# Kernel optimization log

Hardware: AMD Instinct MI355X
Metric: run time of the kernel (lower is better)

## Reference

```python
import jax, jax.numpy as jnp
import numpy as np

B, S, D, H, L, V = 32, 100, 1024, 16, 2, 32000
DF = 4 * D
EPS_LN = 1e-5
EPS_Q = 1e-6


def _ln(x, scale, bias):
    mu = jnp.mean(x, axis=-1, keepdims=True)
    var = jnp.mean(jnp.square(x - mu), axis=-1, keepdims=True)
    return (x - mu) * jax.lax.rsqrt(var + EPS_LN) * scale + bias


def setup_inputs() -> dict:
    key = jax.random.key(0)
    ks = jax.random.split(key, 20)
    sd = 0.02
    inp = {
        "x": jax.random.randint(ks[0], (B, S), 0, V),
        "emb": jax.random.normal(ks[1], (V, D), jnp.float32) * sd,
        "pos_emb": jax.random.normal(ks[2], (100, D), jnp.float32) * sd,
        "qkv_w": jax.random.normal(ks[3], (L, 3 * D, D), jnp.float32) * sd,
        "qkv_b": jnp.zeros((L, 3 * D), jnp.float32),
        "out_w": jax.random.normal(ks[4], (L, D, D), jnp.float32) * sd,
        "out_b": jnp.zeros((L, D), jnp.float32),
        "ln1_s": jnp.ones((L, D), jnp.float32),
        "ln1_b": jnp.zeros((L, D), jnp.float32),
        "ff1_w": jax.random.normal(ks[5], (L, DF, D), jnp.float32) * sd,
        "ff1_b": jnp.zeros((L, DF), jnp.float32),
        "ff2_w": jax.random.normal(ks[6], (L, D, DF), jnp.float32) * sd,
        "ff2_b": jnp.zeros((L, D), jnp.float32),
        "ln2_s": jnp.ones((L, D), jnp.float32),
        "ln2_b": jnp.zeros((L, D), jnp.float32),
        "dec_w": jax.random.normal(ks[7], (V, D), jnp.float32) * sd,
        "dec_b": jnp.zeros((V,), jnp.float32),
    }
    return inp


def reference(x, emb, pos_emb, qkv_w, qkv_b, out_w, out_b, ln1_s, ln1_b,
              ff1_w, ff1_b, ff2_w, ff2_b, ln2_s, ln2_b, dec_w, dec_b):
    hd = D // H
    h = emb[x] + pos_emb[:S][None, :, :]  # [B,S,D]
    for l in range(L):
        qkv = h @ qkv_w[l].T + qkv_b[l]  # [B,S,3D]
        q, k, v = jnp.split(qkv, 3, axis=-1)
        q = q.reshape(B, S, H, hd).transpose(0, 2, 1, 3)
        k = k.reshape(B, S, H, hd).transpose(0, 2, 1, 3)
        v = v.reshape(B, S, H, hd).transpose(0, 2, 1, 3)
        scores = jnp.einsum('bhqd,bhkd->bhqk', q, k) / jnp.sqrt(jnp.float32(hd))
        attn = jax.nn.softmax(scores, axis=-1)
        ctx = jnp.einsum('bhqk,bhkd->bhqd', attn, v)
        ctx = ctx.transpose(0, 2, 1, 3).reshape(B, S, D)
        attn_out = ctx @ out_w[l].T + out_b[l]
        h = _ln(h + attn_out, ln1_s[l], ln1_b[l])  # post-norm
        ff = jax.nn.gelu(h @ ff1_w[l].T + ff1_b[l], approximate=False) @ ff2_w[l].T + ff2_b[l]
        h = _ln(h + ff, ln2_s[l], ln2_b[l])
    # Ternary decoder (faithful to the original pack/unpack semantics:
    # packed code = q+1; unpack adds x when code==1 (q==0) and subtracts when
    # code==2 (q==+1), i.e. effective weight = {q==0: +1, q==+1: -1, q==-1: 0}).
    g = jnp.mean(jnp.abs(dec_w))
    wq = jnp.clip(jnp.round(dec_w / (g + EPS_Q)), -1.0, 1.0)
    w_eff = jnp.where(wq == 0.0, 1.0, jnp.where(wq == 1.0, -1.0, 0.0)).astype(jnp.float32)
    return h @ w_eff.T + dec_b  # [B,S,V]
```

## Files before the change

### kernel.cpp

```cpp
#include <hip/hip_runtime.h>
#include <hip/hip_bf16.h>
#include <math.h>

#define B_ 32
#define S_ 100
#define D_ 1024
#define H_ 16
#define L_ 2
#define V_ 32000
#define DF_ 4096
#define HD_ 64
#define MPAD 3328

typedef __bf16 bf16x8 __attribute__((ext_vector_type(8)));
typedef float f32x4 __attribute__((ext_vector_type(4)));

__device__ __forceinline__ void async_copy16(const void* g, void* l) {
  __builtin_amdgcn_global_load_lds((const __attribute__((address_space(1))) void*)g,
                                   (__attribute__((address_space(3))) void*)l, 16, 0, 0);
}

__global__ void absmean_kernel(const float* __restrict__ w, double* __restrict__ out) {
  const long long n4 = (long long)V_ * D_ / 4;
  double s = 0.0;
  long long stride = (long long)gridDim.x * blockDim.x;
  for (long long i = (long long)blockIdx.x * blockDim.x + threadIdx.x; i < n4; i += stride) {
    float4 v = ((const float4*)w)[i];
    s += (double)fabsf(v.x) + (double)fabsf(v.y) + (double)fabsf(v.z) + (double)fabsf(v.w);
  }
#pragma unroll
  for (int off = 32; off > 0; off >>= 1) s += __shfl_down(s, off);
  __shared__ double sm[4];
  int lane = threadIdx.x & 63, wv = threadIdx.x >> 6;
  if (lane == 0) sm[wv] = s;
  __syncthreads();
  if (threadIdx.x == 0) atomicAdd(out, sm[0] + sm[1] + sm[2] + sm[3]);
}

__global__ void quantize_kernel(const float* __restrict__ w, const double* __restrict__ gsum,
                                __hip_bfloat16* __restrict__ q) {
  const long long n4 = (long long)V_ * D_ / 4;
  double g = (*gsum) / ((double)V_ * D_) + 1e-6;
  double inv_g = 1.0 / g;
  long long stride = (long long)gridDim.x * blockDim.x;
  for (long long i = (long long)blockIdx.x * blockDim.x + threadIdx.x; i < n4; i += stride) {
    float4 v = ((const float4*)w)[i];
    union { __hip_bfloat16 h[4]; uint2 u; } o;
    float vv[4] = {v.x, v.y, v.z, v.w};
#pragma unroll
    for (int j = 0; j < 4; ++j) {
      double r = rint((double)vv[j] * inv_g);
      r = fmin(1.0, fmax(-1.0, r));
      float w_eff = (r == 0.0) ? 1.0f : ((r == 1.0) ? -1.0f : 0.0f);
      o.h[j] = __float2bfloat16(w_eff);
    }
    ((uint2*)q)[i] = o.u;
  }
}

__global__ void cast_all_kernel(const float* __restrict__ qkv_w, const float* __restrict__ out_w,
                                const float* __restrict__ ff1_w, const float* __restrict__ ff2_w,
                                __hip_bfloat16* __restrict__ qd, __hip_bfloat16* __restrict__ od,
                                __hip_bfloat16* __restrict__ f1d, __hip_bfloat16* __restrict__ f2d) {
  const long long n1 = (long long)2 * 3072 * 1024 / 4;
  const long long n2 = n1 + (long long)2 * 1024 * 1024 / 4;
  const long long n3 = n2 + (long long)2 * 4096 * 1024 / 4;
  const long long n4 = n3 + (long long)2 * 1024 * 4096 / 4;
  long long stride = (long long)gridDim.x * blockDim.x;
  for (long long i = (long long)blockIdx.x * blockDim.x + threadIdx.x; i < n4; i += stride) {
    const float* src; __hip_bfloat16* dst; long long j;
    if (i < n1)      { src = qkv_w; dst = qd;  j = i; }
    else if (i < n2) { src = out_w; dst = od;  j = i - n1; }
    else if (i < n3) { src = ff1_w; dst = f1d; j = i - n2; }
    else             { src = ff2_w; dst = f2d; j = i - n3; }
    float4 v = ((const float4*)src)[j];
    union { __hip_bfloat16 h[4]; uint2 u; } o;
    o.h[0] = __float2bfloat16(v.x);
    o.h[1] = __float2bfloat16(v.y);
    o.h[2] = __float2bfloat16(v.z);
    o.h[3] = __float2bfloat16(v.w);
    ((uint2*)dst)[j] = o.u;
  }
}

__global__ __launch_bounds__(256) void embed_kernel(const int* __restrict__ x,
    const float* __restrict__ emb, const float* __restrict__ pos,
    float* __restrict__ h, __hip_bfloat16* __restrict__ hb) {
  int row = blockIdx.x;
  int s = row % S_;
  int tok = x[row];
  size_t eb = (size_t)tok * D_, pb = (size_t)s * D_, hb0 = (size_t)row * D_;
#pragma unroll
  for (int i = 0; i < 4; ++i) {
    int d = threadIdx.x + i * 256;
    float v = emb[eb + d] + pos[pb + d];
    h[hb0 + d] = v;
    hb[hb0 + d] = __float2bfloat16(v);
  }
}

__device__ __forceinline__ float gelu_exact(float v) {
  return 0.5f * v * (1.0f + erff(v * 0.70710678118654752f));
}

template <int ACT, int OUTBF>
__global__ __launch_bounds__(256) void gemm_bf(const __hip_bfloat16* __restrict__ A,
    const __hip_bfloat16* __restrict__ Bm, const float* __restrict__ bias,
    void* __restrict__ C, void* __restrict__ C2, int M, int N, int K, int lda, int ldb) {
  __shared__ __bf16 As[128 * 64];
  __shared__ __bf16 Bs[128 * 64];
  int tid = threadIdx.x;
  int lane = tid & 63, wid = tid >> 6;
  int wr = wid >> 1, wc = wid & 1;
  int z = blockIdx.z;

  int nwg = gridDim.x * gridDim.y;
  int orig = blockIdx.y * gridDim.x + blockIdx.x;
  int q = nwg >> 3, r = nwg & 7;
  int xcd = orig & 7, local = orig >> 3;
  int wgid = (xcd < r ? xcd * (q + 1) : r * (q + 1) + (xcd - r) * q) + local;
  int row0 = (wgid % gridDim.x) * 128;
  int col0 = (wgid / gridDim.x) * 128;

  const __hip_bfloat16* Az = A + (size_t)z * K;
  const __hip_bfloat16* Bz = Bm + (size_t)z * K;
  int j0 = wid * 2;
  const __hip_bfloat16* Ag0 = Az + (size_t)(row0 + j0 * 16 + (lane >> 2)) * lda + (lane & 3) * 8;
  const __hip_bfloat16* Ag1 = Az + (size_t)(row0 + (j0 + 1) * 16 + (lane >> 2)) * lda + (lane & 3) * 8;
  const __hip_bfloat16* Bg0 = Bz + (size_t)(col0 + j0 * 16 + (lane >> 2)) * ldb + (lane & 3) * 8;
  const __hip_bfloat16* Bg1 = Bz + (size_t)(col0 + (j0 + 1) * 16 + (lane >> 2)) * ldb + (lane & 3) * 8;
  __bf16* Al0 = As + j0 * 512;
  __bf16* Al1 = As + (j0 + 1) * 512;
  __bf16* Bl0 = Bs + j0 * 512;
  __bf16* Bl1 = Bs + (j0 + 1) * 512;

  float bias_v[4];
#pragma unroll
  for (int ni = 0; ni < 4; ++ni)
    bias_v[ni] = (z == 0) ? bias[col0 + wc * 64 + ni * 16 + (lane & 15)] : 0.f;

  f32x4 acc[4][4];
#pragma unroll
  for (int mi = 0; mi < 4; ++mi)
#pragma unroll
    for (int ni = 0; ni < 4; ++ni) acc[mi][ni] = (f32x4){0.f, 0.f, 0.f, 0.f};

  const bf16x8* Asv = reinterpret_cast<const bf16x8*>(As);
  const bf16x8* Bsv = reinterpret_cast<const bf16x8*>(Bs);
  int afr = (wr * 64 + (lane & 15)) * 4 + (lane >> 4);
  int bfr = (wc * 64 + (lane & 15)) * 4 + (lane >> 4);

  for (int k0 = 0; k0 < K; k0 += 64) {
    async_copy16(Ag0, Al0);  async_copy16(Ag0 + 32, (char*)Al0 + 8192);
    async_copy16(Ag1, Al1);  async_copy16(Ag1 + 32, (char*)Al1 + 8192);
    async_copy16(Bg0, Bl0);  async_copy16(Bg0 + 32, (char*)Bl0 + 8192);
    async_copy16(Bg1, Bl1);  async_copy16(Bg1 + 32, (char*)Bl1 + 8192);
    Ag0 += 64; Ag1 += 64; Bg0 += 64; Bg1 += 64;
    __syncthreads();
    bf16x8 af[4][2], bq[4][2];
#pragma unroll
    for (int mi = 0; mi < 4; ++mi)
#pragma unroll
      for (int kk = 0; kk < 2; ++kk) af[mi][kk] = Asv[afr + mi * 64 + kk * 512];
#pragma unroll
    for (int ni = 0; ni < 4; ++ni)
#pragma unroll
      for (int kk = 0; kk < 2; ++kk) bq[ni][kk] = Bsv[bfr + ni * 64 + kk * 512];
#pragma unroll
    for (int mi = 0; mi < 4; ++mi)
#pragma unroll
      for (int ni = 0; ni < 4; ++ni)
#pragma unroll
        for (int kk = 0; kk < 2; ++kk)
          acc[mi][ni] = __builtin_amdgcn_mfma_f32_16x16x32_bf16(af[mi][kk], bq[ni][kk], acc[mi][ni], 0, 0, 0);
    __syncthreads();
  }

  float* Cf = (float*)((z == 0) ? C : C2);
  __hip_bfloat16* Cb = (__hip_bfloat16*)C;
#pragma unroll
  for (int mi = 0; mi < 4; ++mi) {
#pragma unroll
    for (int r2 = 0; r2 < 4; ++r2) {
      size_t m = row0 + wr * 64 + mi * 16 + (lane >> 4) * 4 + r2;
#pragma unroll
      for (int ni = 0; ni < 4; ++ni) {
        size_t n = col0 + wc * 64 + ni * 16 + (lane & 15);
        float v = acc[mi][ni][r2] + bias_v[ni];
        if (ACT == 1) v = gelu_exact(v);
        if (OUTBF) Cb[m * N + n] = __float2bfloat16(v);
        else       Cf[m * N + n] = v;
      }
    }
  }
}

template <int ACT, int OUTBF>
__global__ __launch_bounds__(512, 1) void gemm256(
    const __hip_bfloat16* __restrict__ A, const __hip_bfloat16* __restrict__ Bm,
    const float* __restrict__ bias, void* __restrict__ C,
    int Mreal, int N, int K) {
  extern __shared__ char lds[];
  char* ldsA = lds;
  char* ldsB = lds + 65536;
  const int t = threadIdx.x;
  const int lane = t & 63, wid = t >> 6;
  const int wm = wid >> 2, wn = wid & 3;
  const int NT = K >> 6;

  int nwg = gridDim.x * gridDim.y;
  int orig = blockIdx.y * gridDim.x + blockIdx.x;
  int q = nwg >> 3, r = nwg & 7;
  int xcd = orig & 7, local = orig >> 3;
  int wgid = (xcd < r ? xcd * (q + 1) : r * (q + 1) + (xcd - r) * q) + local;
  int row0 = (wgid % gridDim.x) * 256;
  int col0 = (wgid / gridDim.x) * 256;

  const int rs = t >> 2;
  const int kc = ((((t & 3) << 4) ^ (((t >> 5) & 1) << 5)) >> 1);
  const __hip_bfloat16* Asrc = A + (size_t)(row0 + rs) * K + kc;
  const __hip_bfloat16* Bsrc = Bm + (size_t)(col0 + rs) * K + kc;

#define STAGE_A(b, h, tgt) do { \
    const __hip_bfloat16* _s = Asrc + (size_t)(h) * 128 * K + (tgt) * 64; \
    char* _d = ldsA + (b) * 32768 + (h) * 16384 + t * 16; \
    async_copy16(_s, _d); async_copy16(_s + 32, _d + 8192); } while (0)
#define STAGE_B(b, h, tgt) do { \
    const __hip_bfloat16* _s = Bsrc + (size_t)(h) * 128 * K + (tgt) * 64; \
    char* _d = ldsB + (b) * 32768 + (h) * 16384 + t * 16; \
    async_copy16(_s, _d); async_copy16(_s + 32, _d + 8192); } while (0)
#define SB() __builtin_amdgcn_sched_barrier(0)
#define BAR() __builtin_amdgcn_s_barrier()

  const int sb5 = ((lane >> 3) & 1) << 5;
  const int laneoff = ((lane & 15) << 6) + (((lane >> 4) << 4) ^ sb5);

  f32x4 acc[8][4];
#pragma unroll
  for (int i = 0; i < 8; ++i)
#pragma unroll
    for (int j = 0; j < 4; ++j) acc[i][j] = (f32x4){0.f, 0.f, 0.f, 0.f};

  STAGE_A(0, 0, 0); STAGE_B(0, 0, 0); STAGE_A(0, 1, 0); STAGE_B(0, 1, 0);
  STAGE_B(1, 0, 1); STAGE_A(1, 0, 1);
  asm volatile("s_waitcnt vmcnt(4)" ::: "memory");
  SB(); BAR(); SB();

  bf16x8 a[4][2], b[4][2];
  for (int T = 0; T < NT; ++T) {
    const int bs = T & 1;
    const char* Aw = ldsA + bs * 32768 + wm * 16384 + laneoff;
    const char* Bw = ldsB + bs * 32768 + (wn >> 1) * 16384 + (wn & 1) * 4096 + laneoff;
#pragma unroll
    for (int mi = 0; mi < 4; ++mi)
#pragma unroll
      for (int kk = 0; kk < 2; ++kk)
        a[mi][kk] = *(const bf16x8*)(Aw + mi * 1024 + kk * 8192);
#pragma unroll
    for (int ni = 0; ni < 2; ++ni)
#pragma unroll
      for (int kk = 0; kk < 2; ++kk)
        b[ni][kk] = *(const bf16x8*)(Bw + ni * 1024 + kk * 8192);
    if (T + 1 < NT) STAGE_A(bs ^ 1, 1, T + 1);
    SB(); BAR(); SB();
    __builtin_amdgcn_s_setprio(1);
#pragma unroll
    for (int mi = 0; mi < 4; ++mi)
#pragma unroll
      for (int ni = 0; ni < 2; ++ni)
#pragma unroll
        for (int kk = 0; kk < 2; ++kk)
          acc[mi][ni] = __builtin_amdgcn_mfma_f32_16x16x32_bf16(a[mi][kk], b[ni][kk], acc[mi][ni], 0, 0, 0);
    __builtin_amdgcn_s_setprio(0);
    SB(); BAR(); SB();
#pragma unroll
    for (int ni = 2; ni < 4; ++ni)
#pragma unroll
      for (int kk = 0; kk < 2; ++kk)
        b[ni][kk] = *(const bf16x8*)(Bw + ni * 1024 + kk * 8192);
    if (T + 1 < NT) STAGE_B(bs ^ 1, 1, T + 1);
    SB(); BAR(); SB();
    __builtin_amdgcn_s_setprio(1);
#pragma unroll
    for (int mi = 0; mi < 4; ++mi)
#pragma unroll
      for (int ni = 2; ni < 4; ++ni)
#pragma unroll
        for (int kk = 0; kk < 2; ++kk)
          acc[mi][ni] = __builtin_amdgcn_mfma_f32_16x16x32_bf16(a[mi][kk], b[ni][kk], acc[mi][ni], 0, 0, 0);
    __builtin_amdgcn_s_setprio(0);
    SB(); BAR(); SB();
#pragma unroll
    for (int mi = 0; mi < 4; ++mi)
#pragma unroll
      for (int kk = 0; kk < 2; ++kk)
        a[mi][kk] = *(const bf16x8*)(Aw + (mi + 4) * 1024 + kk * 8192);
    if (T + 2 < NT) STAGE_B(bs, 0, T + 2);
    SB(); BAR(); SB();
    __builtin_amdgcn_s_setprio(1);
#pragma unroll
    for (int mi = 0; mi < 4; ++mi)
#pragma unroll
      for (int ni = 0; ni < 2; ++ni)
#pragma unroll
        for (int kk = 0; kk < 2; ++kk)
          acc[mi + 4][ni] = __builtin_amdgcn_mfma_f32_16x16x32_bf16(a[mi][kk], b[ni][kk], acc[mi + 4][ni], 0, 0, 0);
    __builtin_amdgcn_s_setprio(0);
    SB(); BAR(); SB();
    if (T + 2 < NT) STAGE_A(bs, 0, T + 2);
    if (T < NT - 2) { asm volatile("s_waitcnt vmcnt(4)" ::: "memory"); }
    else            { asm volatile("s_waitcnt vmcnt(0)" ::: "memory"); }
    SB(); BAR(); SB();
    __builtin_amdgcn_s_setprio(1);
#pragma unroll
    for (int mi = 0; mi < 4; ++mi)
#pragma unroll
      for (int ni = 2; ni < 4; ++ni)
#pragma unroll
        for (int kk = 0; kk < 2; ++kk)
          acc[mi + 4][ni] = __builtin_amdgcn_mfma_f32_16x16x32_bf16(a[mi][kk], b[ni][kk], acc[mi + 4][ni], 0, 0, 0);
    __builtin_amdgcn_s_setprio(0);
    SB(); BAR(); SB();
  }
#undef STAGE_A
#undef STAGE_B
#undef SB
#undef BAR

  float bias_v[4];
#pragma unroll
  for (int ni = 0; ni < 4; ++ni)
    bias_v[ni] = bias[col0 + wn * 64 + ni * 16 + (lane & 15)];
  float* Cf = (float*)C;
  __hip_bfloat16* Cb = (__hip_bfloat16*)C;
#pragma unroll
  for (int mi = 0; mi < 8; ++mi) {
#pragma unroll
    for (int r2 = 0; r2 < 4; ++r2) {
      int m = row0 + wm * 128 + mi * 16 + (lane >> 4) * 4 + r2;
      if (m < Mreal) {
#pragma unroll
        for (int ni = 0; ni < 4; ++ni) {
          int n = col0 + wn * 64 + ni * 16 + (lane & 15);
          float v = acc[mi][ni][r2] + bias_v[ni];
          if (ACT == 1) v = gelu_exact(v);
          if (OUTBF) Cb[(size_t)m * N + n] = __float2bfloat16(v);
          else       Cf[(size_t)m * N + n] = v;
        }
      }
    }
  }
}

__global__ __launch_bounds__(128) void attn_kernel(const __hip_bfloat16* __restrict__ qkv,
                                                   __hip_bfloat16* __restrict__ ctx) {
  __shared__ float KV[50][64];
  __shared__ float Sc[100][101];
  int bh = blockIdx.x;
  int b = bh >> 4, hh = bh & 15;
  int tid = threadIdx.x;
  size_t base = (size_t)b * S_ * (3 * D_);
  int hcol = hh * HD_;
  int r = tid;

  float qa[64];
  if (r < 100) {
    const __hip_bfloat16* qp = qkv + base + (size_t)r * (3 * D_) + hcol;
#pragma unroll
    for (int d0 = 0; d0 < 8; ++d0) {
      union { uint4 u; __hip_bfloat16 h[8]; } uu;
      uu.u = *(const uint4*)(qp + d0 * 8);
#pragma unroll
      for (int j = 0; j < 8; ++j) qa[d0 * 8 + j] = __bfloat162float(uu.h[j]);
    }
  }
  for (int tt = 0; tt < 2; ++tt) {
    __syncthreads();
    for (int idx = tid; idx < 400; idx += 128) {
      int j = idx >> 3, d8 = idx & 7;
      union { uint4 u; __hip_bfloat16 h[8]; } uu;
      uu.u = *(const uint4*)(qkv + base + (size_t)(tt * 50 + j) * (3 * D_) + D_ + hcol + d8 * 8);
#pragma unroll
      for (int e = 0; e < 8; ++e) KV[j][d8 * 8 + e] = __bfloat162float(uu.h[e]);
    }
    __syncthreads();
    if (r < 100) {
      for (int j = 0; j < 50; ++j) {
        float s = 0.f;
#pragma unroll
        for (int d0 = 0; d0 < 16; ++d0) {
          float4 kv = *(const float4*)&KV[j][d0 * 4];
          s += qa[d0 * 4 + 0] * kv.x + qa[d0 * 4 + 1] * kv.y +
               qa[d0 * 4 + 2] * kv.z + qa[d0 * 4 + 3] * kv.w;
        }
        Sc[r][tt * 50 + j] = s * 0.125f;
      }
    }
  }
  float inv_sum = 0.f;
  if (r < 100) {
    float mx = -1e30f;
    for (int j = 0; j < 100; ++j) mx = fmaxf(mx, Sc[r][j]);
    float sum = 0.f;
    for (int j = 0; j < 100; ++j) {
      float e = expf(Sc[r][j] - mx);
      Sc[r][j] = e;
      sum += e;
    }
    inv_sum = 1.0f / sum;
  }
  float ca[64];
#pragma unroll
  for (int d = 0; d < 64; ++d) ca[d] = 0.f;
  for (int tt = 0; tt < 2; ++tt) {
    __syncthreads();
    for (int idx = tid; idx < 400; idx += 128) {
      int j = idx >> 3, d8 = idx & 7;
      union { uint4 u; __hip_bfloat16 h[8]; } uu;
      uu.u = *(const uint4*)(qkv + base + (size_t)(tt * 50 + j) * (3 * D_) + 2 * D_ + hcol + d8 * 8);
#pragma unroll
      for (int e = 0; e < 8; ++e) KV[j][d8 * 8 + e] = __bfloat162float(uu.h[e]);
    }
    __syncthreads();
    if (r < 100) {
      for (int j = 0; j < 50; ++j) {
        float p = Sc[r][tt * 50 + j];
#pragma unroll
        for (int d0 = 0; d0 < 16; ++d0) {
          float4 kv = *(const float4*)&KV[j][d0 * 4];
          ca[d0 * 4 + 0] += p * kv.x;
          ca[d0 * 4 + 1] += p * kv.y;
          ca[d0 * 4 + 2] += p * kv.z;
          ca[d0 * 4 + 3] += p * kv.w;
        }
      }
    }
  }
  if (r < 100) {
    __hip_bfloat16* cp = ctx + ((size_t)b * S_ + r) * D_ + hcol;
#pragma unroll
    for (int d = 0; d < 64; ++d) cp[d] = __float2bfloat16(ca[d] * inv_sum);
  }
}

__device__ float block_sum_1024(float v) {
#pragma unroll
  for (int off = 32; off > 0; off >>= 1) v += __shfl_down(v, off);
  __shared__ float sm[4];
  __syncthreads();
  int lane = threadIdx.x & 63, wv = threadIdx.x >> 6;
  if (lane == 0) sm[wv] = v;
  __syncthreads();
  return sm[0] + sm[1] + sm[2] + sm[3];
}

__global__ __launch_bounds__(256) void add_ln_kernel(float* __restrict__ h,
    const float* __restrict__ res, const float* __restrict__ res2,
    const float* __restrict__ scale, const float* __restrict__ bias,
    __hip_bfloat16* __restrict__ hb) {
  size_t b4 = (size_t)blockIdx.x * 256 + threadIdx.x;
  float4 xa = ((const float4*)h)[b4];
  float4 xb = ((const float4*)res)[b4];
  float x[4] = {xa.x + xb.x, xa.y + xb.y, xa.z + xb.z, xa.w + xb.w};
  if (res2) {
    float4 xc = ((const float4*)res2)[b4];
    x[0] += xc.x; x[1] += xc.y; x[2] += xc.z; x[3] += xc.w;
  }
  float s = x[0] + x[1] + x[2] + x[3];
  float mu = block_sum_1024(s) * (1.0f / 1024.0f);
  float v = 0.f;
#pragma unroll
  for (int i = 0; i < 4; ++i) {
    float d = x[i] - mu;
    v += d * d;
  }
  float var = block_sum_1024(v) * (1.0f / 1024.0f);
  float rs = rsqrtf(var + 1e-5f);
  int d0 = threadIdx.x * 4;
  float4 sc = *(const float4*)&scale[d0];
  float4 bi = *(const float4*)&bias[d0];
  float o[4];
  o[0] = (x[0] - mu) * rs * sc.x + bi.x;
  o[1] = (x[1] - mu) * rs * sc.y + bi.y;
  o[2] = (x[2] - mu) * rs * sc.z + bi.z;
  o[3] = (x[3] - mu) * rs * sc.w + bi.w;
  ((float4*)h)[b4] = (float4){o[0], o[1], o[2], o[3]};
  union { __hip_bfloat16 hh[4]; uint2 u; } ob;
#pragma unroll
  for (int i = 0; i < 4; ++i) ob.hh[i] = __float2bfloat16(o[i]);
  ((uint2*)hb)[b4] = ob.u;
}

extern "C" void kernel_launch(void* const* d_in, const int* in_sizes, int n_in,
                              void* d_out, int out_size, void* d_ws, size_t ws_size,
                              hipStream_t stream) {
  const int* x       = (const int*)d_in[0];
  const float* emb   = (const float*)d_in[1];
  const float* pos   = (const float*)d_in[2];
  const float* qkv_w = (const float*)d_in[3];
  const float* qkv_b = (const float*)d_in[4];
  const float* out_w = (const float*)d_in[5];
  const float* out_b = (const float*)d_in[6];
  const float* ln1_s = (const float*)d_in[7];
  const float* ln1_b = (const float*)d_in[8];
  const float* ff1_w = (const float*)d_in[9];
  const float* ff1_b = (const float*)d_in[10];
  const float* ff2_w = (const float*)d_in[11];
  const float* ff2_b = (const float*)d_in[12];
  const float* ln2_s = (const float*)d_in[13];
  const float* ln2_b = (const float*)d_in[14];
  const float* dec_w = (const float*)d_in[15];
  const float* dec_b = (const float*)d_in[16];
  float* out = (float*)d_out;

  char* ws = (char*)d_ws;
  size_t off = 0;
  auto alloc = [&](size_t bytes) { void* p = ws + off; off += (bytes + 255) & ~(size_t)255; return p; };
  double* gsum            = (double*)alloc(256);
  float* h                = (float*)alloc((size_t)3200 * 1024 * 4);
  __hip_bfloat16* h_bf    = (__hip_bfloat16*)alloc((size_t)MPAD * 1024 * 2);
  float* tmp              = (float*)alloc((size_t)3200 * 1024 * 4);
  float* tmp2             = (float*)alloc((size_t)3200 * 1024 * 4);
  __hip_bfloat16* ctx_bf  = (__hip_bfloat16*)alloc((size_t)3200 * 1024 * 2);
  __hip_bfloat16* big_bf  = (__hip_bfloat16*)alloc((size_t)3200 * 4096 * 2);
  __hip_bfloat16* weff    = (__hip_bfloat16*)alloc((size_t)32000 * 1024 * 2);
  __hip_bfloat16* qkvw_bf = (__hip_bfloat16*)alloc((size_t)2 * 3072 * 1024 * 2);
  __hip_bfloat16* outw_bf = (__hip_bfloat16*)alloc((size_t)2 * 1024 * 1024 * 2);
  __hip_bfloat16* ff1w_bf = (__hip_bfloat16*)alloc((size_t)2 * 4096 * 1024 * 2);
  __hip_bfloat16* ff2w_bf = (__hip_bfloat16*)alloc((size_t)2 * 1024 * 4096 * 2);

  hipMemsetAsync(gsum, 0, 256, stream);
  absmean_kernel<<<2048, 256, 0, stream>>>(dec_w, gsum);
  quantize_kernel<<<4096, 256, 0, stream>>>(dec_w, gsum, weff);
  cast_all_kernel<<<4096, 256, 0, stream>>>(qkv_w, out_w, ff1_w, ff2_w,
                                            qkvw_bf, outw_bf, ff1w_bf, ff2w_bf);
  embed_kernel<<<3200, 256, 0, stream>>>(x, emb, pos, h, h_bf);

  const int M = 3200;
  for (int l = 0; l < 2; ++l) {
    gemm256<0, 1><<<dim3(MPAD / 256, 3072 / 256), 512, 131072, stream>>>(
        h_bf, qkvw_bf + (size_t)l * 3072 * 1024, qkv_b + l * 3072, big_bf,
        M, 3072, 1024);
    attn_kernel<<<512, 128, 0, stream>>>(big_bf, ctx_bf);
    gemm_bf<0, 0><<<dim3(M / 128, 1024 / 128, 2), 256, 0, stream>>>(
        ctx_bf, outw_bf + (size_t)l * 1024 * 1024, out_b + l * 1024, tmp, tmp2,
        M, 1024, 512, 1024, 1024);
    add_ln_kernel<<<M, 256, 0, stream>>>(h, tmp, tmp2, ln1_s + l * 1024, ln1_b + l * 1024, h_bf);
    gemm256<1, 1><<<dim3(MPAD / 256, 4096 / 256), 512, 131072, stream>>>(
        h_bf, ff1w_bf + (size_t)l * 4096 * 1024, ff1_b + l * 4096, big_bf,
        M, 4096, 1024);
    gemm_bf<0, 0><<<dim3(M / 128, 1024 / 128, 2), 256, 0, stream>>>(
        big_bf, ff2w_bf + (size_t)l * 1024 * 4096, ff2_b + l * 1024, tmp, tmp2,
        M, 1024, 2048, 4096, 4096);
    add_ln_kernel<<<M, 256, 0, stream>>>(h, tmp, tmp2, ln2_s + l * 1024, ln2_b + l * 1024, h_bf);
  }
  gemm256<0, 0><<<dim3(MPAD / 256, 32000 / 256), 512, 131072, stream>>>(
      h_bf, weff, dec_b, out, M, 32000, 1024);
}
```

Baseline: 911.6 us.

## Replace atomic absmean with partials, merge embed into cast, widen attention blocks

The absmean kernel now writes per-block partial sums, and the quantize kernel reduces them itself, which removes the memset and the double-precision atomics. The embedding kernel is folded into the weight-cast kernel as extra blocks, saving one launch. The attention kernel is launched with 256 threads instead of 128, so K/V loads into shared memory use more threads. Threads with index 100 and above do no compute, so the larger block mostly adds idle waves and register pressure from the 64-float arrays, which may lower occupancy.

```diff
diff --git a/kernel.cpp b/kernel.cpp
--- a/kernel.cpp
+++ b/kernel.cpp
@@ -11,6 +11,7 @@
 #define DF_ 4096
 #define HD_ 64
 #define MPAD 3328
+#define NPART 2048
 
 typedef __bf16 bf16x8 __attribute__((ext_vector_type(8)));
 typedef float f32x4 __attribute__((ext_vector_type(4)));
@@ -20,7 +21,8 @@
                                    (__attribute__((address_space(3))) void*)l, 16, 0, 0);
 }
 
-__global__ void absmean_kernel(const float* __restrict__ w, double* __restrict__ out) {
+__global__ __launch_bounds__(256) void absmean_kernel(const float* __restrict__ w,
+                                                      double* __restrict__ part) {
   const long long n4 = (long long)V_ * D_ / 4;
   double s = 0.0;
   long long stride = (long long)gridDim.x * blockDim.x;
@@ -34,14 +36,27 @@
   int lane = threadIdx.x & 63, wv = threadIdx.x >> 6;
   if (lane == 0) sm[wv] = s;
   __syncthreads();
-  if (threadIdx.x == 0) atomicAdd(out, sm[0] + sm[1] + sm[2] + sm[3]);
-}
-
-__global__ void quantize_kernel(const float* __restrict__ w, const double* __restrict__ gsum,
-                                __hip_bfloat16* __restrict__ q) {
+  if (threadIdx.x == 0) part[blockIdx.x] = sm[0] + sm[1] + sm[2] + sm[3];
+}
+
+__global__ __launch_bounds__(256) void quantize_kernel(const float* __restrict__ w,
+    const double* __restrict__ part, __hip_bfloat16* __restrict__ q) {
+  __shared__ double gsh;
+  {
+    double p = 0.0;
+    for (int i = threadIdx.x; i < NPART; i += 256) p += part[i];
+#pragma unroll
+    for (int off = 32; off > 0; off >>= 1) p += __shfl_down(p, off);
+    __shared__ double sm[4];
+    int lane = threadIdx.x & 63, wv = threadIdx.x >> 6;
+    if (lane == 0) sm[wv] = p;
+    __syncthreads();
+    if (threadIdx.x == 0) gsh = sm[0] + sm[1] + sm[2] + sm[3];
+    __syncthreads();
+  }
+  double g = gsh / ((double)V_ * D_) + 1e-6;
+  double inv_g = 1.0 / g;
   const long long n4 = (long long)V_ * D_ / 4;
-  double g = (*gsum) / ((double)V_ * D_) + 1e-6;
-  double inv_g = 1.0 / g;
   long long stride = (long long)gridDim.x * blockDim.x;
   for (long long i = (long long)blockIdx.x * blockDim.x + threadIdx.x; i < n4; i += stride) {
     float4 v = ((const float4*)w)[i];
@@ -58,16 +73,34 @@
   }
 }
 
-__global__ void cast_all_kernel(const float* __restrict__ qkv_w, const float* __restrict__ out_w,
-                                const float* __restrict__ ff1_w, const float* __restrict__ ff2_w,
-                                __hip_bfloat16* __restrict__ qd, __hip_bfloat16* __restrict__ od,
-                                __hip_bfloat16* __restrict__ f1d, __hip_bfloat16* __restrict__ f2d) {
+__global__ __launch_bounds__(256) void prep_kernel(const int* __restrict__ x,
+    const float* __restrict__ emb, const float* __restrict__ pos,
+    float* __restrict__ h, __hip_bfloat16* __restrict__ hb,
+    const float* __restrict__ qkv_w, const float* __restrict__ out_w,
+    const float* __restrict__ ff1_w, const float* __restrict__ ff2_w,
+    __hip_bfloat16* __restrict__ qd, __hip_bfloat16* __restrict__ od,
+    __hip_bfloat16* __restrict__ f1d, __hip_bfloat16* __restrict__ f2d) {
+  if (blockIdx.x < 3200) {
+    int row = blockIdx.x;
+    int s = row % S_;
+    int tok = x[row];
+    size_t eb = (size_t)tok * D_, pb = (size_t)s * D_, hb0 = (size_t)row * D_;
+#pragma unroll
+    for (int i = 0; i < 4; ++i) {
+      int d = threadIdx.x + i * 256;
+      float v = emb[eb + d] + pos[pb + d];
+      h[hb0 + d] = v;
+      hb[hb0 + d] = __float2bfloat16(v);
+    }
+    return;
+  }
   const long long n1 = (long long)2 * 3072 * 1024 / 4;
   const long long n2 = n1 + (long long)2 * 1024 * 1024 / 4;
   const long long n3 = n2 + (long long)2 * 4096 * 1024 / 4;
   const long long n4 = n3 + (long long)2 * 1024 * 4096 / 4;
-  long long stride = (long long)gridDim.x * blockDim.x;
-  for (long long i = (long long)blockIdx.x * blockDim.x + threadIdx.x; i < n4; i += stride) {
+  long long cb = (long long)(blockIdx.x - 3200);
+  long long stride = (long long)(gridDim.x - 3200) * blockDim.x;
+  for (long long i = cb * blockDim.x + threadIdx.x; i < n4; i += stride) {
     const float* src; __hip_bfloat16* dst; long long j;
     if (i < n1)      { src = qkv_w; dst = qd;  j = i; }
     else if (i < n2) { src = out_w; dst = od;  j = i - n1; }
@@ -83,22 +116,6 @@
   }
 }
 
-__global__ __launch_bounds__(256) void embed_kernel(const int* __restrict__ x,
-    const float* __restrict__ emb, const float* __restrict__ pos,
-    float* __restrict__ h, __hip_bfloat16* __restrict__ hb) {
-  int row = blockIdx.x;
-  int s = row % S_;
-  int tok = x[row];
-  size_t eb = (size_t)tok * D_, pb = (size_t)s * D_, hb0 = (size_t)row * D_;
-#pragma unroll
-  for (int i = 0; i < 4; ++i) {
-    int d = threadIdx.x + i * 256;
-    float v = emb[eb + d] + pos[pb + d];
-    h[hb0 + d] = v;
-    hb[hb0 + d] = __float2bfloat16(v);
-  }
-}
-
 __device__ __forceinline__ float gelu_exact(float v) {
   return 0.5f * v * (1.0f + erff(v * 0.70710678118654752f));
 }
@@ -352,7 +369,7 @@
   }
 }
 
-__global__ __launch_bounds__(128) void attn_kernel(const __hip_bfloat16* __restrict__ qkv,
+__global__ __launch_bounds__(256) void attn_kernel(const __hip_bfloat16* __restrict__ qkv,
                                                    __hip_bfloat16* __restrict__ ctx) {
   __shared__ float KV[50][64];
   __shared__ float Sc[100][101];
@@ -376,7 +393,7 @@
   }
   for (int tt = 0; tt < 2; ++tt) {
     __syncthreads();
-    for (int idx = tid; idx < 400; idx += 128) {
+    for (int idx = tid; idx < 400; idx += 256) {
       int j = idx >> 3, d8 = idx & 7;
       union { uint4 u; __hip_bfloat16 h[8]; } uu;
       uu.u = *(const uint4*)(qkv + base + (size_t)(tt * 50 + j) * (3 * D_) + D_ + hcol + d8 * 8);
@@ -414,7 +431,7 @@
   for (int d = 0; d < 64; ++d) ca[d] = 0.f;
   for (int tt = 0; tt < 2; ++tt) {
     __syncthreads();
-    for (int idx = tid; idx < 400; idx += 128) {
+    for (int idx = tid; idx < 400; idx += 256) {
       int j = idx >> 3, d8 = idx & 7;
       union { uint4 u; __hip_bfloat16 h[8]; } uu;
       uu.u = *(const uint4*)(qkv + base + (size_t)(tt * 50 + j) * (3 * D_) + 2 * D_ + hcol + d8 * 8);
@@ -516,7 +533,7 @@
   char* ws = (char*)d_ws;
   size_t off = 0;
   auto alloc = [&](size_t bytes) { void* p = ws + off; off += (bytes + 255) & ~(size_t)255; return p; };
-  double* gsum            = (double*)alloc(256);
+  double* gpart           = (double*)alloc(NPART * 8);
   float* h                = (float*)alloc((size_t)3200 * 1024 * 4);
   __hip_bfloat16* h_bf    = (__hip_bfloat16*)alloc((size_t)MPAD * 1024 * 2);
   float* tmp              = (float*)alloc((size_t)3200 * 1024 * 4);
@@ -529,19 +546,18 @@
   __hip_bfloat16* ff1w_bf = (__hip_bfloat16*)alloc((size_t)2 * 4096 * 1024 * 2);
   __hip_bfloat16* ff2w_bf = (__hip_bfloat16*)alloc((size_t)2 * 1024 * 4096 * 2);
 
-  hipMemsetAsync(gsum, 0, 256, stream);
-  absmean_kernel<<<2048, 256, 0, stream>>>(dec_w, gsum);
-  quantize_kernel<<<4096, 256, 0, stream>>>(dec_w, gsum, weff);
-  cast_all_kernel<<<4096, 256, 0, stream>>>(qkv_w, out_w, ff1_w, ff2_w,
-                                            qkvw_bf, outw_bf, ff1w_bf, ff2w_bf);
-  embed_kernel<<<3200, 256, 0, stream>>>(x, emb, pos, h, h_bf);
+  absmean_kernel<<<NPART, 256, 0, stream>>>(dec_w, gpart);
+  quantize_kernel<<<4096, 256, 0, stream>>>(dec_w, gpart, weff);
+  prep_kernel<<<3200 + 4096, 256, 0, stream>>>(x, emb, pos, h, h_bf,
+                                               qkv_w, out_w, ff1_w, ff2_w,
+                                               qkvw_bf, outw_bf, ff1w_bf, ff2w_bf);
 
   const int M = 3200;
   for (int l = 0; l < 2; ++l) {
     gemm256<0, 1><<<dim3(MPAD / 256, 3072 / 256), 512, 131072, stream>>>(
         h_bf, qkvw_bf + (size_t)l * 3072 * 1024, qkv_b + l * 3072, big_bf,
         M, 3072, 1024);
-    attn_kernel<<<512, 128, 0, stream>>>(big_bf, ctx_bf);
+    attn_kernel<<<512, 256, 0, stream>>>(big_bf, ctx_bf);
     gemm_bf<0, 0><<<dim3(M / 128, 1024 / 128, 2), 256, 0, stream>>>(
         ctx_bf, outw_bf + (size_t)l * 1024 * 1024, out_b + l * 1024, tmp, tmp2,
         M, 1024, 512, 1024, 1024);
```

Result: faster. 885.4 us, median of 2 (-2.9%).
